# Optimization experiments

Hardware: AMD Instinct MI355X
Metric: run time of the kernel (lower is better)

## Reference

```python
import jax, jax.numpy as jnp
import numpy as np

B, N, D_FEAT = 4, 2048, 3
P = B * N
C_KP, K_PTS, NSAMPLE = 64, 15, 64
RADIUS, WINDOW = 0.2, 0.25
KP_EXTENT = 0.08  # prev_grid_size * sigma
F, H, HID, L = 256, 8, 512, 2
DH = F // H
EPS = 1e-5


def setup_inputs() -> dict:
    key = jax.random.key(0)
    k = jax.random.split(key, 24)
    s = 0.02
    position = jax.random.uniform(k[0], (B, N, 3), jnp.float32)
    feature = jax.random.normal(k[1], (B, N, D_FEAT), jnp.float32)
    # KPConv kernel points: fixed points inside a ball of radius 1.5*KP_EXTENT
    d = jax.random.normal(k[2], (K_PTS, 3))
    d = d / jnp.clip(jnp.linalg.norm(d, axis=1, keepdims=True), 1e-6)
    r = jax.random.uniform(k[3], (K_PTS, 1)) ** (1.0 / 3.0)
    kernel_points = (d * r * 1.5 * KP_EXTENT).astype(jnp.float32)
    return dict(
        position=position,
        feature=feature,
        kernel_points=kernel_points,
        kp_weights=s * jax.random.normal(k[4], (K_PTS, D_FEAT, C_KP), jnp.float32),
        bn_gamma=jnp.ones((C_KP,), jnp.float32),
        bn_beta=jnp.zeros((C_KP,), jnp.float32),
        weightmatrix=jax.random.normal(k[5], (1, C_KP + 3, F), jnp.float32) * s,
        Wq=s * jax.random.normal(k[6], (L, F, F), jnp.float32),
        bq=jnp.zeros((L, F), jnp.float32),
        Wk=s * jax.random.normal(k[7], (L, F, F), jnp.float32),
        bk=jnp.zeros((L, F), jnp.float32),
        Wv=s * jax.random.normal(k[8], (L, F, F), jnp.float32),
        bv=jnp.zeros((L, F), jnp.float32),
        Wo=s * jax.random.normal(k[9], (L, F, F), jnp.float32),
        bo=jnp.zeros((L, F), jnp.float32),
        ln1_g=jnp.ones((L, F), jnp.float32),
        ln1_b=jnp.zeros((L, F), jnp.float32),
        W1=s * jax.random.normal(k[10], (L, F, HID), jnp.float32),
        b1=jnp.zeros((L, HID), jnp.float32),
        W2=s * jax.random.normal(k[11], (L, HID, F), jnp.float32),
        b2=jnp.zeros((L, F), jnp.float32),
        ln2_g=jnp.ones((L, F), jnp.float32),
        ln2_b=jnp.zeros((L, F), jnp.float32),
    )


def _ball_query(position):
    """partial_dense ball query: first NSAMPLE in-radius neighbors per point, fill=P."""
    def one(b, pb):
        d2 = jnp.sum((pb[:, None, :] - pb[None, :, :]) ** 2, -1)      # [N,N]
        within = d2 <= RADIUS ** 2
        # stable argsort puts in-radius indices first, in ascending index order
        order = jnp.argsort(jnp.where(within, 0, 1).astype(jnp.int32), axis=1)[:, :NSAMPLE]
        valid = jnp.arange(NSAMPLE)[None, :] < jnp.sum(within, axis=1)[:, None]
        return jnp.where(valid, order + b * N, P)
    return jax.vmap(one)(jnp.arange(B), position).reshape(P, NSAMPLE)


def _kpconv(pos_flat, feat_flat, idx, kernel_points, kp_weights, bn_gamma, bn_beta):
    pos_pad = jnp.concatenate([pos_flat, jnp.full((1, 3), 1e6, pos_flat.dtype)], 0)
    feat_pad = jnp.concatenate([feat_flat, jnp.zeros((1, feat_flat.shape[1]), feat_flat.dtype)], 0)
    neigh = pos_pad[idx] - pos_flat[:, None, :]                     # [P,NS,3]
    diff = neigh[:, :, None, :] - kernel_points[None, None]         # [P,NS,K,3]
    dist = jnp.sqrt(jnp.sum(diff * diff, -1) + 1e-12)               # [P,NS,K]
    infl = jnp.clip(1.0 - dist / KP_EXTENT, 0.0)                    # linear influence
    nf = feat_pad[idx]                                              # [P,NS,Din]
    wf = jnp.einsum('pnk,pnd->pkd', infl, nf)
    out = jnp.einsum('pkd,kdc->pc', wf, kp_weights)                 # [P,C]
    mu = out.mean(0)
    var = out.var(0)
    out = bn_gamma * (out - mu) * jax.lax.rsqrt(var + EPS) + bn_beta
    return jnp.where(out >= 0, out, 0.2 * out)                      # LeakyReLU(0.2)


def _cluster_mask(position):
    """grid_sample: same-voxel points attend to each other. Returns bool [B,N,N]."""
    start = position.min(axis=1, keepdims=True)
    cell = jnp.floor((position - start) / WINDOW).astype(jnp.int32)
    cid = cell[..., 0] * 4096 + cell[..., 1] * 64 + cell[..., 2]
    return cid[:, :, None] == cid[:, None, :]


def _ln(x, g, b):
    mu = x.mean(-1, keepdims=True)
    v = x.var(-1, keepdims=True)
    return g * (x - mu) * jax.lax.rsqrt(v + EPS) + b


def _enc(x, mask, Wq, bq, Wk, bk, Wv, bv, Wo, bo, g1, be1, W1, bb1, W2, bb2, g2, be2):
    q = (x @ Wq + bq).reshape(B, N, H, DH)
    k = (x @ Wk + bk).reshape(B, N, H, DH)
    v = (x @ Wv + bv).reshape(B, N, H, DH)
    s = jnp.einsum('bihd,bjhd->bhij', q, k) * (1.0 / np.sqrt(DH))
    s = jnp.where(mask[:, None, :, :], s, -1e9)
    p = jax.nn.softmax(s, -1)
    o = jnp.einsum('bhij,bjhd->bihd', p, v).reshape(B, N, F)
    x = _ln(x + o @ Wo + bo, g1, be1)
    h = jax.nn.relu(x @ W1 + bb1) @ W2 + bb2
    return _ln(x + h, g2, be2)


def reference(position, feature, kernel_points, kp_weights, bn_gamma, bn_beta, weightmatrix,
              Wq, bq, Wk, bk, Wv, bv, Wo, bo, ln1_g, ln1_b, W1, b1, W2, b2, ln2_g, ln2_b):
    pos_flat = position.reshape(P, 3)
    feat_flat = feature.reshape(P, D_FEAT)
    idx = _ball_query(position)
    kpf = _kpconv(pos_flat, feat_flat, idx, kernel_points, kp_weights, bn_gamma, bn_beta)
    kpf = kpf.reshape(B, N, C_KP)
    mask = _cluster_mask(position)
    pw = jnp.concatenate([position, kpf], -1)                       # [B,N,C+3]
    emb = jnp.einsum('bnc,cf->bnf', pw, weightmatrix[0])
    for l in range(L):
        emb = _enc(emb, mask, Wq[l], bq[l], Wk[l], bk[l], Wv[l], bv[l], Wo[l], bo[l],
                   ln1_g[l], ln1_b[l], W1[l], b1[l], W2[l], b2[l], ln2_g[l], ln2_b[l])
    return emb
```

## Files before the change

### kernel.cpp

```cpp
#include <hip/hip_runtime.h>
#include <math.h>

#define BATCH 4
#define NPTS  2048
#define PTS   8192
#define NS    64
#define KPTS  15
#define CKP   64
#define FDIM  256
#define HIDD  512
#define NHEAD 8
#define DHEAD 32
#define NLAY  2
#define R2    0.04f
#define KPE   0.08f
#define WIN   0.25f
#define EPSF  1e-5f
#define SCALE 0.17677669529663687f
#define CPITCH 264

typedef __attribute__((ext_vector_type(8))) short          short8;
typedef __attribute__((ext_vector_type(8))) unsigned short ushort8;
typedef __attribute__((ext_vector_type(4))) float          f32x4;

static __device__ __forceinline__ unsigned short f2bf(float f) {
    unsigned int u = __float_as_uint(f);
    unsigned int r = u + 0x7fffu + ((u >> 16) & 1u);
    return (unsigned short)(r >> 16);
}
static __device__ __forceinline__ float b2f(unsigned short u) {
    return __uint_as_float(((unsigned int)u) << 16);
}

__global__ __launch_bounds__(256) void prep_k(
    const float* __restrict__ pos,
    const float* __restrict__ Wq, const float* __restrict__ Wk,
    const float* __restrict__ Wv, const float* __restrict__ Wo,
    const float* __restrict__ W1, const float* __restrict__ W2,
    const float* __restrict__ bq, const float* __restrict__ bk,
    const float* __restrict__ bv,
    unsigned short* __restrict__ wT, float* __restrict__ bqkv,
    int* __restrict__ sorted, int* __restrict__ inv,
    int* __restrict__ offs, int* __restrict__ hist,
    unsigned long long* __restrict__ masks)
{
    __shared__ __align__(16) unsigned char sm[38400];
    int bid = blockIdx.x, tid = threadIdx.x;

    if (bid < 3072) {
        int z = bid >> 8, r = bid & 255;
        int bx = r & 15, by = r >> 4;
        int t = z >> 1, l = z & 1;
        const float* src; unsigned short* dst; int K, N;
        switch (t) {
            case 0: src=Wq+(size_t)l*65536;  dst=wT+(size_t)l*196608;           K=256; N=256; break;
            case 1: src=Wk+(size_t)l*65536;  dst=wT+(size_t)l*196608+65536;     K=256; N=256; break;
            case 2: src=Wv+(size_t)l*65536;  dst=wT+(size_t)l*196608+131072;    K=256; N=256; break;
            case 3: src=Wo+(size_t)l*65536;  dst=wT+393216+(size_t)l*65536;     K=256; N=256; break;
            case 4: src=W1+(size_t)l*131072; dst=wT+524288+(size_t)l*131072;    K=256; N=512; break;
            default:src=W2+(size_t)l*131072; dst=wT+786432+(size_t)l*131072;    K=512; N=256; break;
        }
        int n0 = bx*32, k0 = by*32;
        if (n0 >= N || k0 >= K) return;
        float* ld = (float*)sm;
        #pragma unroll
        for (int i = 0; i < 4; ++i) { int v=tid+i*256; int ty=v>>5, tx=v&31;
            ld[ty*33+tx] = src[(size_t)(k0+ty)*N + n0+tx]; }
        __syncthreads();
        #pragma unroll
        for (int i = 0; i < 4; ++i) { int v=tid+i*256; int ny=v>>5, nk=v&31;
            dst[(size_t)(n0+ny)*K + k0+nk] = f2bf(ld[nk*33+ny]); }
    } else if (bid < 3584) {
        int m_ = bid - 3072;
        int chunk = m_ & 31, b = (m_ >> 5) & 3, qg = m_ >> 7;
        int w = tid >> 6, lane = tid & 63;
        float* qx = (float*)sm; float* qy = qx + 512; float* qz = qy + 512;
        int qbase = qg * 512;
        for (int t = tid; t < 512; t += 256) {
            const float* q = pos + (size_t)(b*NPTS + qbase + t)*3;
            qx[t] = q[0]; qy[t] = q[1]; qz[t] = q[2];
        }
        const float* c = pos + (size_t)(b*NPTS + chunk*64 + lane)*3;
        float cx = c[0], cy = c[1], cz = c[2];
        __syncthreads();
        int q0 = w * 128;
        for (int i = 0; i < 128; ++i) {
            int qi = q0 + i;
            float dx = cx - qx[qi], dy = cy - qy[qi], dz = cz - qz[qi];
            float d2 = dx*dx + dy*dy + dz*dz;
            unsigned long long m = __ballot(d2 <= R2);
            if (lane == 0) masks[(size_t)(b*NPTS + qbase + qi)*32 + chunk] = m;
        }
    } else if (bid < 3588) {
        int b = bid - 3584;
        float* sx = (float*)sm; float* sy = sx + 256; float* sz = sy + 256;
        unsigned char* cid_s = sm + 3072;
        unsigned int* maskc = (unsigned int*)(sm + 5120);
        int* wpfx = (int*)(sm + 21504);
        int* tot  = (int*)(sm + 37888);
        int* off_c= (int*)(sm + 38144);
        float mx=1e30f, my=1e30f, mz=1e30f;
        for (int n = tid; n < NPTS; n += 256) {
            const float* q = pos + ((size_t)b*NPTS + n)*3;
            mx = fminf(mx, q[0]); my = fminf(my, q[1]); mz = fminf(mz, q[2]);
        }
        sx[tid]=mx; sy[tid]=my; sz[tid]=mz; __syncthreads();
        for (int o=128;o;o>>=1){ if(tid<o){sx[tid]=fminf(sx[tid],sx[tid+o]);sy[tid]=fminf(sy[tid],sy[tid+o]);sz[tid]=fminf(sz[tid],sz[tid+o]);} __syncthreads(); }
        float X = sx[0], Y = sy[0], Z = sz[0];
        __syncthreads();
        for (int i = tid; i < 64*64; i += 256) maskc[i] = 0u;
        __syncthreads();
        for (int n = tid; n < NPTS; n += 256) {
            const float* q = pos + ((size_t)b*NPTS + n)*3;
            int cx = (int)floorf((q[0]-X)/WIN);
            int cy = (int)floorf((q[1]-Y)/WIN);
            int cz = (int)floorf((q[2]-Z)/WIN);
            int c = (cx<<4) | (cy<<2) | cz;
            cid_s[n] = (unsigned char)c;
            atomicOr(&maskc[c*64 + (n>>5)], 1u << (n & 31));
        }
        __syncthreads();
        if (tid < 64) {
            int run = 0;
            for (int wd = 0; wd < 64; ++wd) { wpfx[tid*64+wd] = run; run += __popc(maskc[tid*64+wd]); }
            tot[tid] = run;
        }
        __syncthreads();
        if (tid == 0) { int run = 0; for (int c = 0; c < 64; ++c) { off_c[c] = run; run += tot[c]; } }
        __syncthreads();
        if (tid < 64) { hist[b*64+tid] = tot[tid]; offs[b*64+tid] = off_c[tid]; }
        for (int n = tid; n < NPTS; n += 256) {
            int c = cid_s[n];
            int wd = n >> 5;
            int rank = wpfx[c*64+wd] + __popc(maskc[c*64+wd] & ((1u << (n & 31)) - 1u));
            int slot = b*NPTS + off_c[c] + rank;
            int p = b*NPTS + n;
            sorted[slot] = p;
            inv[p] = slot;
        }
    } else {
        int i = (bid - 3588)*256 + tid;
        if (i < 2*768) {
            int l = i / 768, n = i - l*768;
            float v = (n < 256) ? bq[l*256+n] : (n < 512) ? bk[l*256+n-256] : bv[l*256+n-512];
            bqkv[l*768 + n] = v;
        }
    }
}

__global__ __launch_bounds__(256) void kpc_k(
    const float* __restrict__ pos, const float* __restrict__ feat,
    const unsigned long long* __restrict__ masks,
    const float* __restrict__ kpts, const float* __restrict__ kpw,
    float* __restrict__ raw)
{
    __shared__ int   idxs[64][66];
    __shared__ float kpwl[45*64];
    __shared__ float kpl[48];
    __shared__ float wfp[64*181 + 4];

    int tid = threadIdx.x, w = tid >> 6, lane = tid & 63;
    int pb = blockIdx.x * 64;
    int b = pb >> 11;
    int base = b * NPTS;

    for (int t = tid; t < 45*64; t += 256) kpwl[t] = kpw[t];
    if (tid < 45) kpl[tid] = kpts[tid];

    int g = tid >> 5, j = tid & 31;
    for (int pp = 0; pp < 8; ++pp) {
        int lp = pp*8 + g;
        unsigned long long m = masks[(size_t)(pb + lp)*32 + j];
        int cnt = __popcll(m);
        int inc = cnt;
        #pragma unroll
        for (int off = 1; off < 32; off <<= 1) {
            int v = __shfl_up(inc, off, 32);
            if (j >= off) inc += v;
        }
        int pfx = inc - cnt;
        int total = __shfl(inc, 31, 32);
        unsigned long long mm = m; int slot = pfx;
        while (mm && slot < NS) {
            int bit = __ffsll((long long)mm) - 1;
            idxs[lp][slot++] = j*64 + bit;
            mm &= mm - 1;
        }
        int cc = total < NS ? total : NS;
        for (int s = cc + j; s < NS; s += 32) idxs[lp][s] = NPTS;
    }
    __syncthreads();

    float wf[45];
    #pragma unroll
    for (int t = 0; t < 45; ++t) wf[t] = 0.f;
    {
        int p = pb + lane;
        float xi = pos[(size_t)p*3+0], yi = pos[(size_t)p*3+1], zi = pos[(size_t)p*3+2];
        for (int n = w*16; n < w*16 + 16; ++n) {
            int id = idxs[lane][n];
            if (id < NPTS) {
                const float* pq = pos + (size_t)(base + id)*3;
                float rx = pq[0]-xi, ry = pq[1]-yi, rz = pq[2]-zi;
                const float* ff = feat + (size_t)(base + id)*3;
                float g0 = ff[0], g1 = ff[1], g2 = ff[2];
                #pragma unroll
                for (int k = 0; k < KPTS; ++k) {
                    float dx = rx - kpl[k*3+0], dy = ry - kpl[k*3+1], dz = rz - kpl[k*3+2];
                    float dist = sqrtf(dx*dx + dy*dy + dz*dz + 1e-12f);
                    float infl = fmaxf(0.f, 1.0f - dist * (1.0f/KPE));
                    wf[k*3+0] = fmaf(infl, g0, wf[k*3+0]);
                    wf[k*3+1] = fmaf(infl, g1, wf[k*3+1]);
                    wf[k*3+2] = fmaf(infl, g2, wf[k*3+2]);
                }
            }
        }
    }
    #pragma unroll
    for (int t = 0; t < 45; ++t) wfp[lane*181 + t*4 + w] = wf[t];
    __syncthreads();
    for (int i = tid; i < 64*45; i += 256) {
        int p_ = i / 45, t = i - p_*45;
        float* q = &wfp[p_*181 + t*4];
        q[0] = (q[0]+q[1]) + (q[2]+q[3]);
    }
    __syncthreads();
    {
        int c = tid & 63, pg = tid >> 6;
        float kw[45];
        #pragma unroll
        for (int t = 0; t < 45; ++t) kw[t] = kpwl[t*64 + c];
        for (int p0 = 0; p0 < 16; p0 += 4) {
            float a0=0.f, a1=0.f, a2=0.f, a3=0.f;
            int pl = pg*16 + p0;
            #pragma unroll
            for (int t = 0; t < 45; ++t) {
                a0 = fmaf(kw[t], wfp[(pl+0)*181 + t*4], a0);
                a1 = fmaf(kw[t], wfp[(pl+1)*181 + t*4], a1);
                a2 = fmaf(kw[t], wfp[(pl+2)*181 + t*4], a2);
                a3 = fmaf(kw[t], wfp[(pl+3)*181 + t*4], a3);
            }
            raw[(size_t)(pb + pl+0)*CKP + c] = a0;
            raw[(size_t)(pb + pl+1)*CKP + c] = a1;
            raw[(size_t)(pb + pl+2)*CKP + c] = a2;
            raw[(size_t)(pb + pl+3)*CKP + c] = a3;
        }
    }
}

__global__ void bn_stats_k(const float* __restrict__ raw, float* __restrict__ stats)
{
    int c = blockIdx.x, tid = threadIdx.x;
    float s = 0.f, q = 0.f;
    for (int p = tid; p < PTS; p += 256) { float v = raw[p*CKP + c]; s += v; q += v*v; }
    __shared__ float sh[256], sh2[256];
    sh[tid]=s; sh2[tid]=q; __syncthreads();
    for (int o = 128; o; o >>= 1) { if (tid < o) { sh[tid]+=sh[tid+o]; sh2[tid]+=sh2[tid+o]; } __syncthreads(); }
    if (tid == 0) { stats[c] = sh[0]; stats[CKP + c] = sh2[0]; }
}

__global__ void embed_k(const float* __restrict__ pos, const float* __restrict__ raw,
                        const float* __restrict__ stats, const float* __restrict__ gamma,
                        const float* __restrict__ beta, const float* __restrict__ Wm,
                        const int* __restrict__ inv,
                        float* __restrict__ xs, unsigned short* __restrict__ xsb)
{
    int p = blockIdx.x, tid = threadIdx.x;
    __shared__ float pw[67];
    if (tid < 3) pw[tid] = pos[p*3 + tid];
    else if (tid < 67) {
        int c = tid - 3;
        float mu  = stats[c] * (1.0f/PTS);
        float var = stats[CKP+c] * (1.0f/PTS) - mu*mu;
        float v = raw[p*CKP + c];
        float h = gamma[c] * (v - mu) * rsqrtf(var + EPSF) + beta[c];
        pw[tid] = h >= 0.f ? h : 0.2f * h;
    }
    __syncthreads();
    float acc = 0.f;
    for (int c = 0; c < 67; ++c) acc += pw[c] * Wm[c*FDIM + tid];
    int slot = inv[p];
    xs[(size_t)slot*FDIM + tid] = acc;
    xsb[(size_t)slot*FDIM + tid] = f2bf(acc);
}

template<int ACT, int LNM, int MR>
__global__ __launch_bounds__(256) void bgemm256_k(
    const unsigned short* __restrict__ A, const unsigned short* __restrict__ Wt,
    const float* __restrict__ bias, const float* __restrict__ R,
    const float* __restrict__ g, const float* __restrict__ be,
    const int* __restrict__ sorted,
    float* __restrict__ Cf, unsigned short* __restrict__ Cb,
    int Nc, int K)
{
    __shared__ unsigned short As[MR*16*72];
    __shared__ unsigned short Bs[256*72];
    __shared__ float red_s[4][32], red_q[4][32];
    int tid = threadIdx.x;
    int l = tid & 63, wc = tid >> 6;
    int lr = l & 15, lk = l >> 4;
    int bm = blockIdx.y * (MR*16), bn = blockIdx.x * 256;

    f32x4 acc[MR][4] = {};

    for (int k0 = 0; k0 < K; k0 += 64) {
        __syncthreads();
        #pragma unroll
        for (int i = 0; i < MR/2; ++i) {
            int id = tid + i*256;
            int row = id >> 3, seg = id & 7;
            *(ushort8*)&As[row*72 + seg*8] =
                *(const ushort8*)&A[(size_t)(bm + row)*K + k0 + seg*8];
        }
        #pragma unroll
        for (int i = 0; i < 8; ++i) {
            int id = tid + i*256;
            int row = id >> 3, seg = id & 7;
            *(ushort8*)&Bs[row*72 + seg*8] =
                *(const ushort8*)&Wt[(size_t)(bn + row)*K + k0 + seg*8];
        }
        __syncthreads();
        #pragma unroll
        for (int kk = 0; kk < 64; kk += 32) {
            short8 a[MR], b[4];
            #pragma unroll
            for (int mi = 0; mi < MR; ++mi)
                a[mi] = *(const short8*)&As[(mi*16 + lr)*72 + kk + lk*8];
            #pragma unroll
            for (int ni = 0; ni < 4; ++ni)
                b[ni] = *(const short8*)&Bs[(wc*64 + ni*16 + lr)*72 + kk + lk*8];
            #pragma unroll
            for (int mi = 0; mi < MR; ++mi)
                #pragma unroll
                for (int ni = 0; ni < 4; ++ni)
                    acc[mi][ni] = __builtin_amdgcn_mfma_f32_16x16x32_bf16(
                        a[mi], b[ni], acc[mi][ni], 0, 0, 0);
        }
    }

    #pragma unroll
    for (int mi = 0; mi < MR; ++mi) {
        #pragma unroll
        for (int r = 0; r < 4; ++r) {
            int row = bm + mi*16 + lk*4 + r;
            #pragma unroll
            for (int ni = 0; ni < 4; ++ni) {
                int col = bn + wc*64 + ni*16 + lr;
                float v = acc[mi][ni][r] + bias[col];
                if (R) v += R[(size_t)row*Nc + col];
                if (ACT == 1) v = v > 0.f ? v : 0.f;
                acc[mi][ni][r] = v;
            }
        }
    }

    if (LNM == 0) {
        #pragma unroll
        for (int mi = 0; mi < MR; ++mi)
            #pragma unroll
            for (int r = 0; r < 4; ++r) {
                int row = bm + mi*16 + lk*4 + r;
                #pragma unroll
                for (int ni = 0; ni < 4; ++ni) {
                    int col = bn + wc*64 + ni*16 + lr;
                    if (Cf) Cf[(size_t)row*Nc + col] = acc[mi][ni][r];
                    if (Cb) Cb[(size_t)row*Nc + col] = f2bf(acc[mi][ni][r]);
                }
            }
    } else {
        #pragma unroll
        for (int mi = 0; mi < 2; ++mi) {
            #pragma unroll
            for (int r = 0; r < 4; ++r) {
                float ps = 0.f, pq = 0.f;
                #pragma unroll
                for (int ni = 0; ni < 4; ++ni) { float v = acc[mi][ni][r]; ps += v; pq += v*v; }
                ps += __shfl_xor(ps, 1);  pq += __shfl_xor(pq, 1);
                ps += __shfl_xor(ps, 2);  pq += __shfl_xor(pq, 2);
                ps += __shfl_xor(ps, 4);  pq += __shfl_xor(pq, 4);
                ps += __shfl_xor(ps, 8);  pq += __shfl_xor(pq, 8);
                if (lr == 0) {
                    int rl = mi*16 + lk*4 + r;
                    red_s[wc][rl] = ps;
                    red_q[wc][rl] = pq;
                }
            }
        }
        __syncthreads();
        #pragma unroll
        for (int mi = 0; mi < 2; ++mi) {
            #pragma unroll
            for (int r = 0; r < 4; ++r) {
                int rl = mi*16 + lk*4 + r;
                float s = red_s[0][rl] + red_s[1][rl] + red_s[2][rl] + red_s[3][rl];
                float q = red_q[0][rl] + red_q[1][rl] + red_q[2][rl] + red_q[3][rl];
                float mu  = s * (1.0f/FDIM);
                float var = q * (1.0f/FDIM) - mu*mu;
                float rs  = rsqrtf(var + EPSF);
                int row = bm + rl;
                #pragma unroll
                for (int ni = 0; ni < 4; ++ni) {
                    int col = wc*64 + ni*16 + lr;
                    float o = g[col]*(acc[mi][ni][r]-mu)*rs + be[col];
                    if (LNM == 2) Cf[(size_t)sorted[row]*FDIM + col] = o;
                    else          Cf[(size_t)row*FDIM + col] = o;
                    if (Cb) Cb[(size_t)row*FDIM + col] = f2bf(o);
                }
            }
        }
    }
}

template<int FINAL>
__global__ __launch_bounds__(256) void ffn_k(
    const unsigned short* __restrict__ A,
    const unsigned short* __restrict__ W1T,
    const float* __restrict__ b1,
    const unsigned short* __restrict__ W2T,
    const float* __restrict__ b2,
    const float* __restrict__ R,
    const float* __restrict__ g, const float* __restrict__ be,
    const int* __restrict__ sorted,
    float* __restrict__ Cf, unsigned short* __restrict__ Cb)
{
    __shared__ unsigned short As[32*264];
    __shared__ unsigned short Bs1[64*264];
    __shared__ unsigned short Bs2[256*72];
    __shared__ unsigned short Hs[32*72];
    __shared__ float red_s[4][32], red_q[4][32];

    int tid = threadIdx.x;
    int l = tid & 63, wc = tid >> 6;
    int lr = l & 15, lk = l >> 4;
    int bm = blockIdx.x * 32;

    #pragma unroll
    for (int i = 0; i < 4; ++i) {
        int id = tid + i*256;
        int row = id >> 5, seg = id & 31;
        *(ushort8*)&As[row*264 + seg*8] =
            *(const ushort8*)&A[(size_t)(bm + row)*FDIM + seg*8];
    }

    f32x4 acc[2][4] = {};

    for (int hc = 0; hc < 8; ++hc) {
        __syncthreads();
        #pragma unroll
        for (int i = 0; i < 8; ++i) {
            int id = tid + i*256;
            int row = id >> 5, seg = id & 31;
            *(ushort8*)&Bs1[row*264 + seg*8] =
                *(const ushort8*)&W1T[(size_t)(hc*64 + row)*FDIM + seg*8];
        }
        #pragma unroll
        for (int i = 0; i < 8; ++i) {
            int id = tid + i*256;
            int row = id >> 3, seg = id & 7;
            *(ushort8*)&Bs2[row*72 + seg*8] =
                *(const ushort8*)&W2T[(size_t)row*HIDD + hc*64 + seg*8];
        }
        __syncthreads();

        f32x4 h[2] = {};
        #pragma unroll
        for (int kk = 0; kk < 256; kk += 32) {
            short8 bfr = *(const short8*)&Bs1[(wc*16 + lr)*264 + kk + lk*8];
            #pragma unroll
            for (int mi = 0; mi < 2; ++mi) {
                short8 a = *(const short8*)&As[(mi*16 + lr)*264 + kk + lk*8];
                h[mi] = __builtin_amdgcn_mfma_f32_16x16x32_bf16(a, bfr, h[mi], 0, 0, 0);
            }
        }
        #pragma unroll
        for (int mi = 0; mi < 2; ++mi)
            #pragma unroll
            for (int r = 0; r < 4; ++r) {
                int row = mi*16 + lk*4 + r;
                int hcol = wc*16 + lr;
                float v = h[mi][r] + b1[hc*64 + hcol];
                v = v > 0.f ? v : 0.f;
                Hs[row*72 + hcol] = f2bf(v);
            }
        __syncthreads();

        #pragma unroll
        for (int kk = 0; kk < 64; kk += 32) {
            short8 pa[2], wb[4];
            #pragma unroll
            for (int mi = 0; mi < 2; ++mi)
                pa[mi] = *(const short8*)&Hs[(mi*16 + lr)*72 + kk + lk*8];
            #pragma unroll
            for (int ni = 0; ni < 4; ++ni)
                wb[ni] = *(const short8*)&Bs2[(wc*64 + ni*16 + lr)*72 + kk + lk*8];
            #pragma unroll
            for (int mi = 0; mi < 2; ++mi)
                #pragma unroll
                for (int ni = 0; ni < 4; ++ni)
                    acc[mi][ni] = __builtin_amdgcn_mfma_f32_16x16x32_bf16(
                        pa[mi], wb[ni], acc[mi][ni], 0, 0, 0);
        }
    }

    #pragma unroll
    for (int mi = 0; mi < 2; ++mi) {
        #pragma unroll
        for (int r = 0; r < 4; ++r) {
            int row = bm + mi*16 + lk*4 + r;
            #pragma unroll
            for (int ni = 0; ni < 4; ++ni) {
                int col = wc*64 + ni*16 + lr;
                acc[mi][ni][r] += b2[col] + R[(size_t)row*FDIM + col];
            }
        }
    }
    #pragma unroll
    for (int mi = 0; mi < 2; ++mi) {
        #pragma unroll
        for (int r = 0; r < 4; ++r) {
            float ps = 0.f, pq = 0.f;
            #pragma unroll
            for (int ni = 0; ni < 4; ++ni) { float v = acc[mi][ni][r]; ps += v; pq += v*v; }
            ps += __shfl_xor(ps, 1);  pq += __shfl_xor(pq, 1);
            ps += __shfl_xor(ps, 2);  pq += __shfl_xor(pq, 2);
            ps += __shfl_xor(ps, 4);  pq += __shfl_xor(pq, 4);
            ps += __shfl_xor(ps, 8);  pq += __shfl_xor(pq, 8);
            if (lr == 0) {
                int rl = mi*16 + lk*4 + r;
                red_s[wc][rl] = ps;
                red_q[wc][rl] = pq;
            }
        }
    }
    __syncthreads();
    #pragma unroll
    for (int mi = 0; mi < 2; ++mi) {
        #pragma unroll
        for (int r = 0; r < 4; ++r) {
            int rl = mi*16 + lk*4 + r;
            float s = red_s[0][rl] + red_s[1][rl] + red_s[2][rl] + red_s[3][rl];
            float q = red_q[0][rl] + red_q[1][rl] + red_q[2][rl] + red_q[3][rl];
            float mu  = s * (1.0f/FDIM);
            float var = q * (1.0f/FDIM) - mu*mu;
            float rs  = rsqrtf(var + EPSF);
            int row = bm + rl;
            #pragma unroll
            for (int ni = 0; ni < 4; ++ni) {
                int col = wc*64 + ni*16 + lr;
                float o = g[col]*(acc[mi][ni][r]-mu)*rs + be[col];
                if (FINAL) Cf[(size_t)sorted[row]*FDIM + col] = o;
                else       Cf[(size_t)row*FDIM + col] = o;
                if (Cb) Cb[(size_t)row*FDIM + col] = f2bf(o);
            }
        }
    }
}

__global__ __launch_bounds__(512) void attn_k(
    const unsigned short* __restrict__ qkv, const int* __restrict__ offs,
    const int* __restrict__ hist, unsigned short* __restrict__ o)
{
    int cci = blockIdx.x, b = blockIdx.y;
    int Mc = hist[b*64 + cci];
    if (Mc == 0) return;
    int off = b*NPTS + offs[b*64 + cci];
    __shared__ unsigned short Kl[64*CPITCH];
    __shared__ unsigned short Vl[64*CPITCH];
    __shared__ unsigned short Pl[8][64*72];
    int tid = threadIdx.x;

    if (Mc <= 64) {
        #pragma unroll
        for (int it = 0; it < 4; ++it) {
            int id = tid + it*512;
            int key = id >> 5, ch8 = (id & 31)*8;
            ushort8 kv, vv;
            if (key < Mc) {
                kv = *(const ushort8*)&qkv[(size_t)(off+key)*768 + 256 + ch8];
                vv = *(const ushort8*)&qkv[(size_t)(off+key)*768 + 512 + ch8];
            } else {
                kv = (ushort8)0; vv = (ushort8)0;
            }
            *(ushort8*)&Kl[key*CPITCH + ch8] = kv;
            *(ushort8*)&Vl[key*CPITCH + ch8] = vv;
        }
        __syncthreads();

        int w = tid >> 6, l = tid & 63;
        int h = w;
        int lr = l & 15, lk = l >> 4;

        f32x4 s[4][4] = {};
        short8 a[4], bb[4];
        #pragma unroll
        for (int mi = 0; mi < 4; ++mi) {
            int rg = off + mi*16 + lr;
            if (rg > PTS-1) rg = PTS-1;
            a[mi] = *(const short8*)&qkv[(size_t)rg*768 + h*32 + lk*8];
        }
        #pragma unroll
        for (int ni = 0; ni < 4; ++ni)
            bb[ni] = *(const short8*)&Kl[(ni*16+lr)*CPITCH + h*32 + lk*8];
        #pragma unroll
        for (int mi = 0; mi < 4; ++mi)
            #pragma unroll
            for (int ni = 0; ni < 4; ++ni)
                s[mi][ni] = __builtin_amdgcn_mfma_f32_16x16x32_bf16(a[mi], bb[ni], s[mi][ni], 0, 0, 0);

        unsigned short* Pw = Pl[w];
        float invl[4][4];
        #pragma unroll
        for (int mi = 0; mi < 4; ++mi) {
            #pragma unroll
            for (int r = 0; r < 4; ++r) {
                int row = mi*16 + lk*4 + r;
                float sv[4]; float mx = -1e30f;
                #pragma unroll
                for (int ni = 0; ni < 4; ++ni) {
                    int col = ni*16 + lr;
                    float x = s[mi][ni][r] * SCALE;
                    sv[ni] = (col < Mc) ? x : -1e30f;
                    mx = fmaxf(mx, sv[ni]);
                }
                mx = fmaxf(mx, __shfl_xor(mx, 1));
                mx = fmaxf(mx, __shfl_xor(mx, 2));
                mx = fmaxf(mx, __shfl_xor(mx, 4));
                mx = fmaxf(mx, __shfl_xor(mx, 8));
                float ls = 0.f;
                #pragma unroll
                for (int ni = 0; ni < 4; ++ni) {
                    float e = __expf(sv[ni] - mx);
                    ls += e;
                    Pw[row*72 + ni*16 + lr] = f2bf(e);
                }
                ls += __shfl_xor(ls, 1);
                ls += __shfl_xor(ls, 2);
                ls += __shfl_xor(ls, 4);
                ls += __shfl_xor(ls, 8);
                invl[mi][r] = 1.0f / ls;
            }
        }

        f32x4 oacc[4][2] = {};
        #pragma unroll
        for (int ks = 0; ks < 2; ++ks) {
            short8 bv[2];
            #pragma unroll
            for (int db = 0; db < 2; ++db) {
                short8 t;
                #pragma unroll
                for (int e = 0; e < 8; ++e)
                    t[e] = (short)Vl[(ks*32 + lk*8 + e)*CPITCH + h*32 + db*16 + lr];
                bv[db] = t;
            }
            #pragma unroll
            for (int mi = 0; mi < 4; ++mi) {
                short8 pa = *(const short8*)&Pw[(mi*16+lr)*72 + ks*32 + lk*8];
                #pragma unroll
                for (int db = 0; db < 2; ++db)
                    oacc[mi][db] = __builtin_amdgcn_mfma_f32_16x16x32_bf16(pa, bv[db], oacc[mi][db], 0, 0, 0);
            }
        }

        #pragma unroll
        for (int mi = 0; mi < 4; ++mi)
            #pragma unroll
            for (int db = 0; db < 2; ++db)
                #pragma unroll
                for (int r = 0; r < 4; ++r) {
                    int row = mi*16 + lk*4 + r;
                    if (row < Mc)
                        o[(size_t)(off+row)*FDIM + h*32 + db*16 + lr] =
                            f2bf(oacc[mi][db][r] * invl[mi][r]);
                }
    } else {
        for (int task = tid; task < Mc*NHEAD; task += 512) {
            int row = task >> 3, h = task & 7;
            float qr[DHEAD];
            #pragma unroll
            for (int d = 0; d < DHEAD; ++d)
                qr[d] = b2f(qkv[(size_t)(off+row)*768 + h*32 + d]);
            float m = -3e38f, lsum = 0.f, acc[DHEAD];
            #pragma unroll
            for (int d = 0; d < DHEAD; ++d) acc[d] = 0.f;
            for (int j = 0; j < Mc; ++j) {
                float dot = 0.f;
                #pragma unroll
                for (int d = 0; d < DHEAD; ++d)
                    dot += qr[d] * b2f(qkv[(size_t)(off+j)*768 + 256 + h*32 + d]);
                float sc = dot * SCALE;
                float mn = fmaxf(m, sc);
                float aa = __expf(m - mn);
                float e  = __expf(sc - mn);
                lsum = lsum*aa + e;
                #pragma unroll
                for (int d = 0; d < DHEAD; ++d)
                    acc[d] = acc[d]*aa + e * b2f(qkv[(size_t)(off+j)*768 + 512 + h*32 + d]);
                m = mn;
            }
            float inv = 1.0f / lsum;
            #pragma unroll
            for (int d = 0; d < DHEAD; ++d)
                o[(size_t)(off+row)*FDIM + h*32 + d] = f2bf(acc[d]*inv);
        }
    }
}

extern "C" void kernel_launch(void* const* d_in, const int* in_sizes, int n_in,
                              void* d_out, int out_size, void* d_ws, size_t ws_size,
                              hipStream_t stream)
{
    (void)in_sizes; (void)n_in; (void)out_size; (void)ws_size;
    const float* pos  = (const float*)d_in[0];
    const float* feat = (const float*)d_in[1];
    const float* kpts = (const float*)d_in[2];
    const float* kpw  = (const float*)d_in[3];
    const float* bn_g = (const float*)d_in[4];
    const float* bn_b = (const float*)d_in[5];
    const float* Wm   = (const float*)d_in[6];
    const float* Wq   = (const float*)d_in[7];
    const float* bq   = (const float*)d_in[8];
    const float* Wk   = (const float*)d_in[9];
    const float* bk   = (const float*)d_in[10];
    const float* Wv   = (const float*)d_in[11];
    const float* bv   = (const float*)d_in[12];
    const float* Wo   = (const float*)d_in[13];
    const float* bo   = (const float*)d_in[14];
    const float* g1   = (const float*)d_in[15];
    const float* be1  = (const float*)d_in[16];
    const float* W1   = (const float*)d_in[17];
    const float* bb1  = (const float*)d_in[18];
    const float* W2   = (const float*)d_in[19];
    const float* bb2  = (const float*)d_in[20];
    const float* g2   = (const float*)d_in[21];
    const float* be2  = (const float*)d_in[22];

    char* ws = (char*)d_ws;
    const size_t MB = 1024*1024;
    float* raw    = (float*)(ws + 0);
    unsigned long long* masks = (unsigned long long*)(ws + 2*MB);
    float* stats  = (float*)(ws + 4*MB);
    int*   hist   = (int*)(ws + 4*MB + 4096);
    int*   offs   = hist + 256;
    int*   sorted = (int*)(ws + 4*MB + 16384);
    int*   inv    = sorted + PTS;
    float* xs   = (float*)(ws + 5*MB);
    float* x2   = (float*)(ws + 13*MB);
    unsigned short* xsb   = (unsigned short*)(ws + 21*MB);
    unsigned short* x2b   = (unsigned short*)(ws + 25*MB);
    unsigned short* qkvb  = (unsigned short*)(ws + 29*MB);
    unsigned short* attnb = (unsigned short*)(ws + 41*MB);
    unsigned short* wT    = (unsigned short*)(ws + 45*MB);
    float*          bqkv  = (float*)(ws + 47*MB);

    prep_k<<<3594, 256, 0, stream>>>(pos, Wq, Wk, Wv, Wo, W1, W2, bq, bk, bv,
                                     wT, bqkv, sorted, inv, offs, hist, masks);
    kpc_k<<<PTS/64, 256, 0, stream>>>(pos, feat, masks, kpts, kpw, raw);
    bn_stats_k<<<CKP, 256, 0, stream>>>(raw, stats);
    embed_k<<<PTS, 256, 0, stream>>>(pos, raw, stats, bn_g, bn_b, Wm, inv, xs, xsb);

    for (int l = 0; l < NLAY; ++l) {
        const unsigned short* W1T_l = wT + 524288 + (size_t)l*131072;
        const unsigned short* W2T_l = wT + 786432 + (size_t)l*131072;
        bgemm256_k<0,0,4><<<dim3(3, PTS/64), 256, 0, stream>>>(
            xsb, wT + (size_t)l*196608, bqkv + l*768, nullptr, nullptr, nullptr, nullptr,
            nullptr, qkvb, 768, FDIM);
        attn_k<<<dim3(64, BATCH), 512, 0, stream>>>(qkvb, offs, hist, attnb);
        bgemm256_k<0,1,2><<<dim3(1, PTS/32), 256, 0, stream>>>(
            attnb, wT + 393216 + (size_t)l*65536, bo + l*FDIM, xs,
            g1 + l*FDIM, be1 + l*FDIM, nullptr, x2, x2b, FDIM, FDIM);
        if (l == NLAY-1)
            ffn_k<1><<<PTS/32, 256, 0, stream>>>(
                x2b, W1T_l, bb1 + l*HIDD, W2T_l, bb2 + l*FDIM, x2,
                g2 + l*FDIM, be2 + l*FDIM, sorted, (float*)d_out, nullptr);
        else
            ffn_k<0><<<PTS/32, 256, 0, stream>>>(
                x2b, W1T_l, bb1 + l*HIDD, W2T_l, bb2 + l*FDIM, x2,
                g2 + l*FDIM, be2 + l*FDIM, nullptr, xs, xsb);
    }
}
```

Measured before the change: 224.3 us.

## Fuse attention with output projection, residual add and LayerNorm per cluster

The per-cluster attention kernel now keeps its output tile in shared memory and applies the Wo projection, bias, residual add and LayerNorm in the same block. It writes x2 and its bf16 copy directly, removing the separate projection GEMM launch and the round trip of the attention output through global memory. The cost is that each cluster block pads its rows to 64 and reloads all of Wo, and work now follows the uneven cluster sizes with one block per cluster. The generic GEMM is trimmed to a bias-only bf16-output variant.

```diff
diff --git a/kernel.cpp b/kernel.cpp
--- a/kernel.cpp
+++ b/kernel.cpp
@@ -284,18 +284,15 @@
     xsb[(size_t)slot*FDIM + tid] = f2bf(acc);
 }
 
-template<int ACT, int LNM, int MR>
+template<int ACT, int MR>
 __global__ __launch_bounds__(256) void bgemm256_k(
     const unsigned short* __restrict__ A, const unsigned short* __restrict__ Wt,
-    const float* __restrict__ bias, const float* __restrict__ R,
-    const float* __restrict__ g, const float* __restrict__ be,
-    const int* __restrict__ sorted,
-    float* __restrict__ Cf, unsigned short* __restrict__ Cb,
+    const float* __restrict__ bias,
+    unsigned short* __restrict__ Cb,
     int Nc, int K)
 {
     __shared__ unsigned short As[MR*16*72];
     __shared__ unsigned short Bs[256*72];
-    __shared__ float red_s[4][32], red_q[4][32];
     int tid = threadIdx.x;
     int l = tid & 63, wc = tid >> 6;
     int lr = l & 15, lk = l >> 4;
@@ -347,67 +344,261 @@
             for (int ni = 0; ni < 4; ++ni) {
                 int col = bn + wc*64 + ni*16 + lr;
                 float v = acc[mi][ni][r] + bias[col];
-                if (R) v += R[(size_t)row*Nc + col];
                 if (ACT == 1) v = v > 0.f ? v : 0.f;
-                acc[mi][ni][r] = v;
-            }
-        }
-    }
-
-    if (LNM == 0) {
-        #pragma unroll
-        for (int mi = 0; mi < MR; ++mi)
+                Cb[(size_t)row*Nc + col] = f2bf(v);
+            }
+        }
+    }
+}
+
+__global__ __launch_bounds__(512) void attn2_k(
+    const unsigned short* __restrict__ qkv, const unsigned short* __restrict__ WoT,
+    const float* __restrict__ bo, const float* __restrict__ xs,
+    const float* __restrict__ g, const float* __restrict__ be,
+    const int* __restrict__ offs, const int* __restrict__ hist,
+    float* __restrict__ x2, unsigned short* __restrict__ x2b)
+{
+    int cci = blockIdx.x, b = blockIdx.y;
+    int Mc = hist[b*64 + cci];
+    if (Mc == 0) return;
+    int off = b*NPTS + offs[b*64 + cci];
+
+    __shared__ unsigned short Kl[64*CPITCH];
+    __shared__ unsigned short Vl[64*CPITCH];
+    __shared__ unsigned short Pl[8][64*72];
+
+    unsigned short* Ol = Kl;
+    unsigned short* Bs = &Pl[0][0];
+    float* red_s = (float*)Vl;
+    float* red_q = red_s + 512;
+
+    int tid = threadIdx.x;
+    int w = tid >> 6, l = tid & 63;
+    int lr = l & 15, lk = l >> 4;
+
+    for (int r0 = 0; r0 < Mc; r0 += 64) {
+        int nr = (Mc - r0) < 64 ? (Mc - r0) : 64;
+
+        if (Mc <= 64) {
+            #pragma unroll
+            for (int it = 0; it < 4; ++it) {
+                int id = tid + it*512;
+                int key = id >> 5, ch8 = (id & 31)*8;
+                ushort8 kv, vv;
+                if (key < Mc) {
+                    kv = *(const ushort8*)&qkv[(size_t)(off+key)*768 + 256 + ch8];
+                    vv = *(const ushort8*)&qkv[(size_t)(off+key)*768 + 512 + ch8];
+                } else {
+                    kv = (ushort8)0; vv = (ushort8)0;
+                }
+                *(ushort8*)&Kl[key*CPITCH + ch8] = kv;
+                *(ushort8*)&Vl[key*CPITCH + ch8] = vv;
+            }
+            __syncthreads();
+
+            int h = w;
+            f32x4 s[4][4] = {};
+            short8 a[4], bb[4];
+            #pragma unroll
+            for (int mi = 0; mi < 4; ++mi) {
+                int rg = off + mi*16 + lr;
+                if (rg > PTS-1) rg = PTS-1;
+                a[mi] = *(const short8*)&qkv[(size_t)rg*768 + h*32 + lk*8];
+            }
+            #pragma unroll
+            for (int ni = 0; ni < 4; ++ni)
+                bb[ni] = *(const short8*)&Kl[(ni*16+lr)*CPITCH + h*32 + lk*8];
+            #pragma unroll
+            for (int mi = 0; mi < 4; ++mi)
+                #pragma unroll
+                for (int ni = 0; ni < 4; ++ni)
+                    s[mi][ni] = __builtin_amdgcn_mfma_f32_16x16x32_bf16(a[mi], bb[ni], s[mi][ni], 0, 0, 0);
+
+            unsigned short* Pw = Pl[w];
+            float invl[4][4];
+            #pragma unroll
+            for (int mi = 0; mi < 4; ++mi) {
+                #pragma unroll
+                for (int r = 0; r < 4; ++r) {
+                    int row = mi*16 + lk*4 + r;
+                    float sv[4]; float mx = -1e30f;
+                    #pragma unroll
+                    for (int ni = 0; ni < 4; ++ni) {
+                        int col = ni*16 + lr;
+                        float x = s[mi][ni][r] * SCALE;
+                        sv[ni] = (col < Mc) ? x : -1e30f;
+                        mx = fmaxf(mx, sv[ni]);
+                    }
+                    mx = fmaxf(mx, __shfl_xor(mx, 1));
+                    mx = fmaxf(mx, __shfl_xor(mx, 2));
+                    mx = fmaxf(mx, __shfl_xor(mx, 4));
+                    mx = fmaxf(mx, __shfl_xor(mx, 8));
+                    float ls = 0.f;
+                    #pragma unroll
+                    for (int ni = 0; ni < 4; ++ni) {
+                        float e = __expf(sv[ni] - mx);
+                        ls += e;
+                        Pw[row*72 + ni*16 + lr] = f2bf(e);
+                    }
+                    ls += __shfl_xor(ls, 1);
+                    ls += __shfl_xor(ls, 2);
+                    ls += __shfl_xor(ls, 4);
+                    ls += __shfl_xor(ls, 8);
+                    invl[mi][r] = 1.0f / ls;
+                }
+            }
+
+            f32x4 oacc[4][2] = {};
+            #pragma unroll
+            for (int ks = 0; ks < 2; ++ks) {
+                short8 bv[2];
+                #pragma unroll
+                for (int db = 0; db < 2; ++db) {
+                    short8 t;
+                    #pragma unroll
+                    for (int e = 0; e < 8; ++e)
+                        t[e] = (short)Vl[(ks*32 + lk*8 + e)*CPITCH + h*32 + db*16 + lr];
+                    bv[db] = t;
+                }
+                #pragma unroll
+                for (int mi = 0; mi < 4; ++mi) {
+                    short8 pa = *(const short8*)&Pw[(mi*16+lr)*72 + ks*32 + lk*8];
+                    #pragma unroll
+                    for (int db = 0; db < 2; ++db)
+                        oacc[mi][db] = __builtin_amdgcn_mfma_f32_16x16x32_bf16(pa, bv[db], oacc[mi][db], 0, 0, 0);
+                }
+            }
+            __syncthreads();
+            #pragma unroll
+            for (int mi = 0; mi < 4; ++mi)
+                #pragma unroll
+                for (int db = 0; db < 2; ++db)
+                    #pragma unroll
+                    for (int r = 0; r < 4; ++r) {
+                        int row = mi*16 + lk*4 + r;
+                        Ol[row*CPITCH + h*32 + db*16 + lr] =
+                            f2bf(oacc[mi][db][r] * invl[mi][r]);
+                    }
+        } else {
+            __syncthreads();
+            for (int task = tid; task < nr*NHEAD; task += 512) {
+                int row = task >> 3, h = task & 7;
+                float qr[DHEAD];
+                #pragma unroll
+                for (int d = 0; d < DHEAD; ++d)
+                    qr[d] = b2f(qkv[(size_t)(off+r0+row)*768 + h*32 + d]);
+                float m = -3e38f, lsum = 0.f, acc[DHEAD];
+                #pragma unroll
+                for (int d = 0; d < DHEAD; ++d) acc[d] = 0.f;
+                for (int jj = 0; jj < Mc; ++jj) {
+                    float dot = 0.f;
+                    #pragma unroll
+                    for (int d = 0; d < DHEAD; ++d)
+                        dot += qr[d] * b2f(qkv[(size_t)(off+jj)*768 + 256 + h*32 + d]);
+                    float sc = dot * SCALE;
+                    float mn = fmaxf(m, sc);
+                    float aa = __expf(m - mn);
+                    float e  = __expf(sc - mn);
+                    lsum = lsum*aa + e;
+                    #pragma unroll
+                    for (int d = 0; d < DHEAD; ++d)
+                        acc[d] = acc[d]*aa + e * b2f(qkv[(size_t)(off+jj)*768 + 512 + h*32 + d]);
+                    m = mn;
+                }
+                float inv = 1.0f / lsum;
+                #pragma unroll
+                for (int d = 0; d < DHEAD; ++d)
+                    Ol[row*CPITCH + h*32 + d] = f2bf(acc[d]*inv);
+            }
+        }
+        __syncthreads();
+
+        f32x4 acc2[4][2] = {};
+        for (int k0 = 0; k0 < 256; k0 += 64) {
+            #pragma unroll
+            for (int i = 0; i < 4; ++i) {
+                int id = tid + i*512;
+                int rown = id >> 3, seg = id & 7;
+                *(ushort8*)&Bs[rown*72 + seg*8] =
+                    *(const ushort8*)&WoT[(size_t)rown*FDIM + k0 + seg*8];
+            }
+            __syncthreads();
+            #pragma unroll
+            for (int kk = 0; kk < 64; kk += 32) {
+                short8 a2[4], b2r[2];
+                #pragma unroll
+                for (int mi = 0; mi < 4; ++mi)
+                    a2[mi] = *(const short8*)&Ol[(mi*16+lr)*CPITCH + k0 + kk + lk*8];
+                #pragma unroll
+                for (int ni = 0; ni < 2; ++ni)
+                    b2r[ni] = *(const short8*)&Bs[(w*32 + ni*16 + lr)*72 + kk + lk*8];
+                #pragma unroll
+                for (int mi = 0; mi < 4; ++mi)
+                    #pragma unroll
+                    for (int ni = 0; ni < 2; ++ni)
+                        acc2[mi][ni] = __builtin_amdgcn_mfma_f32_16x16x32_bf16(
+                            a2[mi], b2r[ni], acc2[mi][ni], 0, 0, 0);
+            }
+            __syncthreads();
+        }
+
+        #pragma unroll
+        for (int mi = 0; mi < 4; ++mi) {
             #pragma unroll
             for (int r = 0; r < 4; ++r) {
-                int row = bm + mi*16 + lk*4 + r;
-                #pragma unroll
-                for (int ni = 0; ni < 4; ++ni) {
-                    int col = bn + wc*64 + ni*16 + lr;
-                    if (Cf) Cf[(size_t)row*Nc + col] = acc[mi][ni][r];
-                    if (Cb) Cb[(size_t)row*Nc + col] = f2bf(acc[mi][ni][r]);
+                int row = mi*16 + lk*4 + r;
+                int srow = off + r0 + row;
+                if (srow > PTS-1) srow = PTS-1;
+                #pragma unroll
+                for (int ni = 0; ni < 2; ++ni) {
+                    int col = w*32 + ni*16 + lr;
+                    acc2[mi][ni][r] += bo[col] + xs[(size_t)srow*FDIM + col];
                 }
             }
-    } else {
-        #pragma unroll
-        for (int mi = 0; mi < 2; ++mi) {
+        }
+        #pragma unroll
+        for (int mi = 0; mi < 4; ++mi) {
             #pragma unroll
             for (int r = 0; r < 4; ++r) {
                 float ps = 0.f, pq = 0.f;
                 #pragma unroll
-                for (int ni = 0; ni < 4; ++ni) { float v = acc[mi][ni][r]; ps += v; pq += v*v; }
+                for (int ni = 0; ni < 2; ++ni) { float v = acc2[mi][ni][r]; ps += v; pq += v*v; }
                 ps += __shfl_xor(ps, 1);  pq += __shfl_xor(pq, 1);
                 ps += __shfl_xor(ps, 2);  pq += __shfl_xor(pq, 2);
                 ps += __shfl_xor(ps, 4);  pq += __shfl_xor(pq, 4);
                 ps += __shfl_xor(ps, 8);  pq += __shfl_xor(pq, 8);
                 if (lr == 0) {
-                    int rl = mi*16 + lk*4 + r;
-                    red_s[wc][rl] = ps;
-                    red_q[wc][rl] = pq;
+                    int row = mi*16 + lk*4 + r;
+                    red_s[w*64 + row] = ps;
+                    red_q[w*64 + row] = pq;
                 }
             }
         }
         __syncthreads();
         #pragma unroll
-        for (int mi = 0; mi < 2; ++mi) {
+        for (int mi = 0; mi < 4; ++mi) {
             #pragma unroll
             for (int r = 0; r < 4; ++r) {
-                int rl = mi*16 + lk*4 + r;
-                float s = red_s[0][rl] + red_s[1][rl] + red_s[2][rl] + red_s[3][rl];
-                float q = red_q[0][rl] + red_q[1][rl] + red_q[2][rl] + red_q[3][rl];
+                int row = mi*16 + lk*4 + r;
+                float s = 0.f, q = 0.f;
+                #pragma unroll
+                for (int ww = 0; ww < 8; ++ww) { s += red_s[ww*64 + row]; q += red_q[ww*64 + row]; }
                 float mu  = s * (1.0f/FDIM);
                 float var = q * (1.0f/FDIM) - mu*mu;
                 float rs  = rsqrtf(var + EPSF);
-                int row = bm + rl;
-                #pragma unroll
-                for (int ni = 0; ni < 4; ++ni) {
-                    int col = wc*64 + ni*16 + lr;
-                    float o = g[col]*(acc[mi][ni][r]-mu)*rs + be[col];
-                    if (LNM == 2) Cf[(size_t)sorted[row]*FDIM + col] = o;
-                    else          Cf[(size_t)row*FDIM + col] = o;
-                    if (Cb) Cb[(size_t)row*FDIM + col] = f2bf(o);
+                if (row < nr) {
+                    int srow = off + r0 + row;
+                    #pragma unroll
+                    for (int ni = 0; ni < 2; ++ni) {
+                        int col = w*32 + ni*16 + lr;
+                        float o = g[col]*(acc2[mi][ni][r]-mu)*rs + be[col];
+                        x2[(size_t)srow*FDIM + col] = o;
+                        x2b[(size_t)srow*FDIM + col] = f2bf(o);
+                    }
                 }
             }
         }
+        __syncthreads();
     }
 }
 
@@ -552,156 +743,6 @@
                 else       Cf[(size_t)row*FDIM + col] = o;
                 if (Cb) Cb[(size_t)row*FDIM + col] = f2bf(o);
             }
-        }
-    }
-}
-
-__global__ __launch_bounds__(512) void attn_k(
-    const unsigned short* __restrict__ qkv, const int* __restrict__ offs,
-    const int* __restrict__ hist, unsigned short* __restrict__ o)
-{
-    int cci = blockIdx.x, b = blockIdx.y;
-    int Mc = hist[b*64 + cci];
-    if (Mc == 0) return;
-    int off = b*NPTS + offs[b*64 + cci];
-    __shared__ unsigned short Kl[64*CPITCH];
-    __shared__ unsigned short Vl[64*CPITCH];
-    __shared__ unsigned short Pl[8][64*72];
-    int tid = threadIdx.x;
-
-    if (Mc <= 64) {
-        #pragma unroll
-        for (int it = 0; it < 4; ++it) {
-            int id = tid + it*512;
-            int key = id >> 5, ch8 = (id & 31)*8;
-            ushort8 kv, vv;
-            if (key < Mc) {
-                kv = *(const ushort8*)&qkv[(size_t)(off+key)*768 + 256 + ch8];
-                vv = *(const ushort8*)&qkv[(size_t)(off+key)*768 + 512 + ch8];
-            } else {
-                kv = (ushort8)0; vv = (ushort8)0;
-            }
-            *(ushort8*)&Kl[key*CPITCH + ch8] = kv;
-            *(ushort8*)&Vl[key*CPITCH + ch8] = vv;
-        }
-        __syncthreads();
-
-        int w = tid >> 6, l = tid & 63;
-        int h = w;
-        int lr = l & 15, lk = l >> 4;
-
-        f32x4 s[4][4] = {};
-        short8 a[4], bb[4];
-        #pragma unroll
-        for (int mi = 0; mi < 4; ++mi) {
-            int rg = off + mi*16 + lr;
-            if (rg > PTS-1) rg = PTS-1;
-            a[mi] = *(const short8*)&qkv[(size_t)rg*768 + h*32 + lk*8];
-        }
-        #pragma unroll
-        for (int ni = 0; ni < 4; ++ni)
-            bb[ni] = *(const short8*)&Kl[(ni*16+lr)*CPITCH + h*32 + lk*8];
-        #pragma unroll
-        for (int mi = 0; mi < 4; ++mi)
-            #pragma unroll
-            for (int ni = 0; ni < 4; ++ni)
-                s[mi][ni] = __builtin_amdgcn_mfma_f32_16x16x32_bf16(a[mi], bb[ni], s[mi][ni], 0, 0, 0);
-
-        unsigned short* Pw = Pl[w];
-        float invl[4][4];
-        #pragma unroll
-        for (int mi = 0; mi < 4; ++mi) {
-            #pragma unroll
-            for (int r = 0; r < 4; ++r) {
-                int row = mi*16 + lk*4 + r;
-                float sv[4]; float mx = -1e30f;
-                #pragma unroll
-                for (int ni = 0; ni < 4; ++ni) {
-                    int col = ni*16 + lr;
-                    float x = s[mi][ni][r] * SCALE;
-                    sv[ni] = (col < Mc) ? x : -1e30f;
-                    mx = fmaxf(mx, sv[ni]);
-                }
-                mx = fmaxf(mx, __shfl_xor(mx, 1));
-                mx = fmaxf(mx, __shfl_xor(mx, 2));
-                mx = fmaxf(mx, __shfl_xor(mx, 4));
-                mx = fmaxf(mx, __shfl_xor(mx, 8));
-                float ls = 0.f;
-                #pragma unroll
-                for (int ni = 0; ni < 4; ++ni) {
-                    float e = __expf(sv[ni] - mx);
-                    ls += e;
-                    Pw[row*72 + ni*16 + lr] = f2bf(e);
-                }
-                ls += __shfl_xor(ls, 1);
-                ls += __shfl_xor(ls, 2);
-                ls += __shfl_xor(ls, 4);
-                ls += __shfl_xor(ls, 8);
-                invl[mi][r] = 1.0f / ls;
-            }
-        }
-
-        f32x4 oacc[4][2] = {};
-        #pragma unroll
-        for (int ks = 0; ks < 2; ++ks) {
-            short8 bv[2];
-            #pragma unroll
-            for (int db = 0; db < 2; ++db) {
-                short8 t;
-                #pragma unroll
-                for (int e = 0; e < 8; ++e)
-                    t[e] = (short)Vl[(ks*32 + lk*8 + e)*CPITCH + h*32 + db*16 + lr];
-                bv[db] = t;
-            }
-            #pragma unroll
-            for (int mi = 0; mi < 4; ++mi) {
-                short8 pa = *(const short8*)&Pw[(mi*16+lr)*72 + ks*32 + lk*8];
-                #pragma unroll
-                for (int db = 0; db < 2; ++db)
-                    oacc[mi][db] = __builtin_amdgcn_mfma_f32_16x16x32_bf16(pa, bv[db], oacc[mi][db], 0, 0, 0);
-            }
-        }
-
-        #pragma unroll
-        for (int mi = 0; mi < 4; ++mi)
-            #pragma unroll
-            for (int db = 0; db < 2; ++db)
-                #pragma unroll
-                for (int r = 0; r < 4; ++r) {
-                    int row = mi*16 + lk*4 + r;
-                    if (row < Mc)
-                        o[(size_t)(off+row)*FDIM + h*32 + db*16 + lr] =
-                            f2bf(oacc[mi][db][r] * invl[mi][r]);
-                }
-    } else {
-        for (int task = tid; task < Mc*NHEAD; task += 512) {
-            int row = task >> 3, h = task & 7;
-            float qr[DHEAD];
-            #pragma unroll
-            for (int d = 0; d < DHEAD; ++d)
-                qr[d] = b2f(qkv[(size_t)(off+row)*768 + h*32 + d]);
-            float m = -3e38f, lsum = 0.f, acc[DHEAD];
-            #pragma unroll
-            for (int d = 0; d < DHEAD; ++d) acc[d] = 0.f;
-            for (int j = 0; j < Mc; ++j) {
-                float dot = 0.f;
-                #pragma unroll
-                for (int d = 0; d < DHEAD; ++d)
-                    dot += qr[d] * b2f(qkv[(size_t)(off+j)*768 + 256 + h*32 + d]);
-                float sc = dot * SCALE;
-                float mn = fmaxf(m, sc);
-                float aa = __expf(m - mn);
-                float e  = __expf(sc - mn);
-                lsum = lsum*aa + e;
-                #pragma unroll
-                for (int d = 0; d < DHEAD; ++d)
-                    acc[d] = acc[d]*aa + e * b2f(qkv[(size_t)(off+j)*768 + 512 + h*32 + d]);
-                m = mn;
-            }
-            float inv = 1.0f / lsum;
-            #pragma unroll
-            for (int d = 0; d < DHEAD; ++d)
-                o[(size_t)(off+row)*FDIM + h*32 + d] = f2bf(acc[d]*inv);
         }
     }
 }
@@ -749,7 +790,6 @@
     unsigned short* xsb   = (unsigned short*)(ws + 21*MB);
     unsigned short* x2b   = (unsigned short*)(ws + 25*MB);
     unsigned short* qkvb  = (unsigned short*)(ws + 29*MB);
-    unsigned short* attnb = (unsigned short*)(ws + 41*MB);
     unsigned short* wT    = (unsigned short*)(ws + 45*MB);
     float*          bqkv  = (float*)(ws + 47*MB);
 
@@ -762,13 +802,11 @@
     for (int l = 0; l < NLAY; ++l) {
         const unsigned short* W1T_l = wT + 524288 + (size_t)l*131072;
         const unsigned short* W2T_l = wT + 786432 + (size_t)l*131072;
-        bgemm256_k<0,0,4><<<dim3(3, PTS/64), 256, 0, stream>>>(
-            xsb, wT + (size_t)l*196608, bqkv + l*768, nullptr, nullptr, nullptr, nullptr,
-            nullptr, qkvb, 768, FDIM);
-        attn_k<<<dim3(64, BATCH), 512, 0, stream>>>(qkvb, offs, hist, attnb);
-        bgemm256_k<0,1,2><<<dim3(1, PTS/32), 256, 0, stream>>>(
-            attnb, wT + 393216 + (size_t)l*65536, bo + l*FDIM, xs,
-            g1 + l*FDIM, be1 + l*FDIM, nullptr, x2, x2b, FDIM, FDIM);
+        bgemm256_k<0,4><<<dim3(3, PTS/64), 256, 0, stream>>>(
+            xsb, wT + (size_t)l*196608, bqkv + l*768, qkvb, 768, FDIM);
+        attn2_k<<<dim3(64, BATCH), 512, 0, stream>>>(
+            qkvb, wT + 393216 + (size_t)l*65536, bo + l*FDIM, xs,
+            g1 + l*FDIM, be1 + l*FDIM, offs, hist, x2, x2b);
         if (l == NLAY-1)
             ffn_k<1><<<PTS/32, 256, 0, stream>>>(
                 x2b, W1T_l, bb1 + l*HIDD, W2T_l, bb2 + l*FDIM, x2,
```

New measurement: 210.0 us. 1.07x faster.
